# Optimization experiments

Measured on AMD Instinct MI355X. Metric: run time of the kernel, lower is better.

The kernel has to match this reference:

```python
import jax, jax.numpy as jnp
import numpy as np

N, I, H = 16, 128, 128
B, T = 16, 512


def setup_inputs() -> dict:
    key = jax.random.key(0)
    ks = jax.random.split(key, 6)
    stdv = 1.0 / np.sqrt(H)
    return {
        "x": jax.random.normal(ks[0], (B, T, N * I), dtype=jnp.float32),
        "h_0": jax.random.normal(ks[1], (1, B, N * H), dtype=jnp.float32),
        "weight_ih": jax.random.uniform(ks[2], (N, 3 * H, I), jnp.float32, -stdv, stdv),
        "weight_hh": jax.random.uniform(ks[3], (N, 3 * H, H), jnp.float32, -stdv, stdv),
        "bias_ih": jax.random.uniform(ks[4], (N, 3 * H), jnp.float32, -stdv, stdv),
        "bias_hh": jax.random.uniform(ks[5], (N, 3 * H), jnp.float32, -stdv, stdv),
    }


def reference(x, h_0, weight_ih, weight_hh, bias_ih, bias_hh):
    # x: [B, T, N*I] (batch_first)
    b, t, _ = x.shape
    xr = x.reshape(b, t, N, I)
    # Pre-compute all input projections: [B, T, N, 3H]
    gates_x = jnp.einsum('btni,ngi->btng', xr, weight_ih) + bias_ih[None, None]
    h0 = h_0[0].reshape(b, N, H)  # [B, N, H]

    def step(h, gx):
        # h: [B, N, H]; gx: [B, N, 3H]
        gates_h = jnp.einsum('bnh,ngh->bng', h, weight_hh) + bias_hh[None]
        gx_r, gx_z, gx_n = jnp.split(gx, 3, axis=-1)
        gh_r, gh_z, gh_n = jnp.split(gates_h, 3, axis=-1)
        r = jax.nn.sigmoid(gx_r + gh_r)
        z = jax.nn.sigmoid(gx_z + gh_z)
        n = jnp.tanh(gx_n + r * gh_n)
        h_new = (1 - z) * n + z * h
        return h_new, h_new

    # scan over time: gates_x -> [T, B, N, 3H]
    h_last, hs = jax.lax.scan(step, h0, jnp.swapaxes(gates_x, 0, 1))
    output = jnp.swapaxes(hs, 0, 1).reshape(b, t, N * H)  # [B, T, N*H]
    h_n = h_last.reshape(1, b, N * H)
    return output, h_n
```

## Files before the change

### kernel.cpp

```cpp
#include <hip/hip_runtime.h>
#include <cstdint>
#include <cmath>

#define N_HEADS 16
#define I_DIM 128
#define H_DIM 128
#define B_SZ 16
#define T_SZ 512
#define G3 384
#define OUT_HN_OFFSET ((size_t)B_SZ * T_SZ * (N_HEADS * H_DIM))
#define CHUNK 8
#define NCHUNK (T_SZ / CHUNK)
#define HPAD 160

typedef __attribute__((ext_vector_type(8))) short bf16x8;
typedef __attribute__((ext_vector_type(4))) float f32x4;

static __device__ __forceinline__ unsigned short f2bf(float f) {
  unsigned int u = __float_as_uint(f);
  unsigned int r = (u + 0x7FFFu + ((u >> 16) & 1u)) >> 16;
  return (unsigned short)r;
}
static __device__ __forceinline__ float bf2f(unsigned short s) {
  return __uint_as_float((unsigned int)s << 16);
}
static __device__ __forceinline__ uint2 pack4(float4 v) {
  uint2 p;
  p.x = (unsigned int)f2bf(v.x) | ((unsigned int)f2bf(v.y) << 16);
  p.y = (unsigned int)f2bf(v.z) | ((unsigned int)f2bf(v.w) << 16);
  return p;
}
static __device__ __forceinline__ bf16x8 pack8(float4 a, float4 b) {
  union { uint2 u[2]; bf16x8 v; } r;
  r.u[0] = pack4(a);
  r.u[1] = pack4(b);
  return r.v;
}

__global__ __launch_bounds__(256, 1) void gru_fused_kernel(
    const float* __restrict__ x, const float* __restrict__ h0,
    const float* __restrict__ w_ih, const float* __restrict__ w_hh,
    const float* __restrict__ b_ih, const float* __restrict__ b_hh,
    float* __restrict__ out) {
  const int b = blockIdx.x >> 4;
  const int n = blockIdx.x & 15;
  const int tid = threadIdx.x;
  const int wave = tid >> 6;
  const int lane = tid & 63;
  const int m16 = lane & 15;
  const int quad = lane >> 4;

  __shared__ __align__(16) unsigned short h2[2][2][HPAD];
  __shared__ __align__(16) float gbuf[2][CHUNK][512];

  bf16x8 wf[6][4];
  {
    const int cb0 = 2 * wave;
    const int cbs[6] = {cb0, 8 + cb0, 16 + cb0, cb0 + 1, 9 + cb0, 17 + cb0};
#pragma unroll
    for (int j = 0; j < 6; ++j) {
      const int g = cbs[j] * 16 + m16;
      const float4* wr = (const float4*)(w_hh + ((size_t)n * G3 + g) * H_DIM);
#pragma unroll
      for (int kt = 0; kt < 4; ++kt)
        wf[j][kt] = pack8(wr[kt * 8 + quad * 2], wr[kt * 8 + quad * 2 + 1]);
    }
  }

  bf16x8 wxf[6][4];
#pragma unroll
  for (int jj = 0; jj < 6; ++jj) {
    const int g = (wave * 6 + jj) * 16 + m16;
    const float4* wr = (const float4*)(w_ih + ((size_t)n * G3 + g) * I_DIM);
#pragma unroll
    for (int kt = 0; kt < 4; ++kt)
      wxf[jj][kt] = pack8(wr[kt * 8 + quad * 2], wr[kt * 8 + quad * 2 + 1]);
  }

  const bool upd = quad < 2;
  const int elem = wave * 32 + quad * 16 + m16;

  float bs_r = 0.f, bs_z = 0.f, bs_n = 0.f, bh_n = 0.f, h_old = 0.f;
  if (upd) {
    bs_r = b_ih[n * G3 + elem] + b_hh[n * G3 + elem];
    bs_z = b_ih[n * G3 + elem + 128] + b_hh[n * G3 + elem + 128];
    bs_n = b_ih[n * G3 + elem + 256];
    bh_n = b_hh[n * G3 + elem + 256];
    h_old = h0[(size_t)b * 2048 + n * H_DIM + elem];
    const unsigned short hh = f2bf(h_old);
    h2[0][0][elem] = hh;
    h2[0][1][elem] = f2bf(h_old - bf2f(hh));
  }

  const float* xrow_base = x + (size_t)b * T_SZ * 2048 + n * I_DIM +
                           (size_t)(m16 & 7) * 2048 + quad * 8;

  float4 pf[8];

#define LOAD_X_CHUNK(c)                                                       \
  {                                                                           \
    const float* xr = xrow_base + (size_t)(c) * CHUNK * 2048;                 \
    _Pragma("unroll") for (int kt = 0; kt < 4; ++kt) {                        \
      pf[kt * 2] = *(const float4*)(xr + kt * 32);                            \
      pf[kt * 2 + 1] = *(const float4*)(xr + kt * 32 + 4);                    \
    }                                                                         \
  }

#define GATES_X_CHUNK(gdst)                                                   \
  {                                                                           \
    bf16x8 af[4];                                                             \
    _Pragma("unroll") for (int kt = 0; kt < 4; ++kt)                          \
        af[kt] = pack8(pf[kt * 2], pf[kt * 2 + 1]);                           \
    _Pragma("unroll") for (int jj = 0; jj < 6; ++jj) {                        \
      f32x4 a = {0.f, 0.f, 0.f, 0.f};                                         \
      _Pragma("unroll") for (int kt = 0; kt < 4; ++kt)                        \
          a = __builtin_amdgcn_mfma_f32_16x16x32_bf16(af[kt], wxf[jj][kt], a, \
                                                      0, 0, 0);               \
      if (quad < 2) {                                                         \
        const int g = (wave * 6 + jj) * 16 + m16;                             \
        const int e4 = (g & 127) * 4 + (g >> 7);                              \
        _Pragma("unroll") for (int r = 0; r < 4; ++r)                         \
            (gdst)[(quad * 4 + r) * 512 + e4] = a[r];                         \
      }                                                                       \
    }                                                                         \
  }

  LOAD_X_CHUNK(0);
  GATES_X_CHUNK(&gbuf[0][0][0]);
  LOAD_X_CHUNK(1);
  __syncthreads();

  float* out_base = out + (size_t)b * T_SZ * 2048 + n * H_DIM;
  float oreg[CHUNK];

  for (int c = 0; c < NCHUNK; ++c) {
    const int gb = c & 1;

    if (c + 1 < NCHUNK) {
      GATES_X_CHUNK(&gbuf[gb ^ 1][0][0]);
      if (c + 2 < NCHUNK) LOAD_X_CHUNK(c + 2);
    }

#pragma unroll
    for (int s = 0; s < CHUNK; ++s) {
      const int rb = s & 1;
      const int wb = rb ^ 1;

      float gxr = 0.f, gxz = 0.f, gxn = 0.f;
      if (upd) {
        const f32x4 g4 = *(const f32x4*)&gbuf[gb][s][elem * 4];
        gxr = g4[0];
        gxz = g4[1];
        gxn = g4[2];
      }

      const unsigned short* hsrc = &h2[rb][m16 & 1][0];
      const bf16x8 av0 = *(const bf16x8*)&hsrc[0 * 32 + quad * 8];
      const bf16x8 av1 = *(const bf16x8*)&hsrc[1 * 32 + quad * 8];
      const bf16x8 av2 = *(const bf16x8*)&hsrc[2 * 32 + quad * 8];
      const bf16x8 av3 = *(const bf16x8*)&hsrc[3 * 32 + quad * 8];

      f32x4 acc[6];
#pragma unroll
      for (int j = 0; j < 6; ++j) acc[j] = (f32x4){0.f, 0.f, 0.f, 0.f};
#pragma unroll
      for (int j = 0; j < 6; ++j)
        acc[j] = __builtin_amdgcn_mfma_f32_16x16x32_bf16(av0, wf[j][0], acc[j],
                                                         0, 0, 0);
#pragma unroll
      for (int j = 0; j < 6; ++j)
        acc[j] = __builtin_amdgcn_mfma_f32_16x16x32_bf16(av1, wf[j][1], acc[j],
                                                         0, 0, 0);
#pragma unroll
      for (int j = 0; j < 6; ++j)
        acc[j] = __builtin_amdgcn_mfma_f32_16x16x32_bf16(av2, wf[j][2], acc[j],
                                                         0, 0, 0);
#pragma unroll
      for (int j = 0; j < 6; ++j)
        acc[j] = __builtin_amdgcn_mfma_f32_16x16x32_bf16(av3, wf[j][3], acc[j],
                                                         0, 0, 0);

      if (upd) {
        const float ghr =
            (quad ? acc[3][0] + acc[3][1] : acc[0][0] + acc[0][1]);
        const float ghz =
            (quad ? acc[4][0] + acc[4][1] : acc[1][0] + acc[1][1]);
        const float ghn0 =
            (quad ? acc[5][0] + acc[5][1] : acc[2][0] + acc[2][1]);
        const float r = 1.f / (1.f + __expf(-(gxr + ghr + bs_r)));
        const float z = 1.f / (1.f + __expf(-(gxz + ghz + bs_z)));
        const float targ = gxn + bs_n + r * (ghn0 + bh_n);
        const float rt = 1.f / (1.f + __expf(-2.f * targ));
        const float nn = 2.f * rt - 1.f;
        const float hn = (1.f - z) * nn + z * h_old;
        const unsigned short hh = f2bf(hn);
        h2[wb][0][elem] = hh;
        h2[wb][1][elem] = f2bf(hn - bf2f(hh));
        h_old = hn;
        oreg[s] = hn;
      }
      __syncthreads();
    }

    if (upd) {
#pragma unroll
      for (int s = 0; s < CHUNK; ++s)
        out_base[(size_t)(c * CHUNK + s) * 2048 + elem] = oreg[s];
    }
  }

  if (upd) {
    out[OUT_HN_OFFSET + (size_t)b * 2048 + n * H_DIM + elem] = h_old;
  }
}

extern "C" void kernel_launch(void* const* d_in, const int* in_sizes, int n_in,
                              void* d_out, int out_size, void* d_ws,
                              size_t ws_size, hipStream_t stream) {
  const float* x    = (const float*)d_in[0];
  const float* h0   = (const float*)d_in[1];
  const float* w_ih = (const float*)d_in[2];
  const float* w_hh = (const float*)d_in[3];
  const float* b_ih = (const float*)d_in[4];
  const float* b_hh = (const float*)d_in[5];
  float* out = (float*)d_out;
  (void)d_ws;

  gru_fused_kernel<<<256, 256, 0, stream>>>(x, h0, w_ih, w_hh, b_ih, b_hh,
                                            out);
}
```

Baseline: 431.6 us.

## Interleave input-projection MFMAs into recurrent steps and use full 16-row tiles

The time chunk grows from 8 to 16 steps, so each input-projection MFMA now uses all 16 rows of the tile instead of duplicating 8. The six projection groups for the next chunk are no longer computed in one burst at the chunk start. Instead they are spread across the first six recurrent steps, issued after the hidden-state MFMAs, so they can fill idle time on the serial critical path. The gate buffer rows are padded to 520 floats to reduce LDS bank conflicts. The cost is a larger shared buffer and more live registers (16 outputs per chunk), which may put pressure on the register file.

After: 446.8 us. 1.04x slower.

```diff
diff --git a/kernel.cpp b/kernel.cpp
--- a/kernel.cpp
+++ b/kernel.cpp
@@ -9,9 +9,10 @@
 #define T_SZ 512
 #define G3 384
 #define OUT_HN_OFFSET ((size_t)B_SZ * T_SZ * (N_HEADS * H_DIM))
-#define CHUNK 8
+#define CHUNK 16
 #define NCHUNK (T_SZ / CHUNK)
 #define HPAD 160
+#define GROWP 520
 
 typedef __attribute__((ext_vector_type(8))) short bf16x8;
 typedef __attribute__((ext_vector_type(4))) float f32x4;
@@ -51,7 +52,7 @@
   const int quad = lane >> 4;
 
   __shared__ __align__(16) unsigned short h2[2][2][HPAD];
-  __shared__ __align__(16) float gbuf[2][CHUNK][512];
+  __shared__ __align__(16) float gbuf[2][CHUNK][GROWP];
 
   bf16x8 wf[6][4];
   {
@@ -93,9 +94,10 @@
   }
 
   const float* xrow_base = x + (size_t)b * T_SZ * 2048 + n * I_DIM +
-                           (size_t)(m16 & 7) * 2048 + quad * 8;
+                           (size_t)m16 * 2048 + quad * 8;
 
   float4 pf[8];
+  bf16x8 af[4];
 
 #define LOAD_X_CHUNK(c)                                                       \
   {                                                                           \
@@ -106,27 +108,35 @@
     }                                                                         \
   }
 
-#define GATES_X_CHUNK(gdst)                                                   \
+#define PACK_AF()                                                             \
   {                                                                           \
-    bf16x8 af[4];                                                             \
     _Pragma("unroll") for (int kt = 0; kt < 4; ++kt)                          \
         af[kt] = pack8(pf[kt * 2], pf[kt * 2 + 1]);                           \
-    _Pragma("unroll") for (int jj = 0; jj < 6; ++jj) {                        \
-      f32x4 a = {0.f, 0.f, 0.f, 0.f};                                         \
-      _Pragma("unroll") for (int kt = 0; kt < 4; ++kt)                        \
-          a = __builtin_amdgcn_mfma_f32_16x16x32_bf16(af[kt], wxf[jj][kt], a, \
-                                                      0, 0, 0);               \
-      if (quad < 2) {                                                         \
-        const int g = (wave * 6 + jj) * 16 + m16;                             \
-        const int e4 = (g & 127) * 4 + (g >> 7);                              \
-        _Pragma("unroll") for (int r = 0; r < 4; ++r)                         \
-            (gdst)[(quad * 4 + r) * 512 + e4] = a[r];                         \
-      }                                                                       \
-    }                                                                         \
+  }
+
+#define GATES_X_GROUP(jj, gdst)                                               \
+  {                                                                           \
+    f32x4 a = {0.f, 0.f, 0.f, 0.f};                                           \
+    a = __builtin_amdgcn_mfma_f32_16x16x32_bf16(af[0], wxf[jj][0], a, 0, 0, 0);\
+    a = __builtin_amdgcn_mfma_f32_16x16x32_bf16(af[1], wxf[jj][1], a, 0, 0, 0);\
+    a = __builtin_amdgcn_mfma_f32_16x16x32_bf16(af[2], wxf[jj][2], a, 0, 0, 0);\
+    a = __builtin_amdgcn_mfma_f32_16x16x32_bf16(af[3], wxf[jj][3], a, 0, 0, 0);\
+    const int g_ = (wave * 6 + (jj)) * 16 + m16;                              \
+    const int e4_ = (g_ & 127) * 4 + (g_ >> 7);                               \
+    (gdst)[(quad * 4 + 0) * GROWP + e4_] = a[0];                              \
+    (gdst)[(quad * 4 + 1) * GROWP + e4_] = a[1];                              \
+    (gdst)[(quad * 4 + 2) * GROWP + e4_] = a[2];                              \
+    (gdst)[(quad * 4 + 3) * GROWP + e4_] = a[3];                              \
   }
 
   LOAD_X_CHUNK(0);
-  GATES_X_CHUNK(&gbuf[0][0][0]);
+  PACK_AF();
+  GATES_X_GROUP(0, &gbuf[0][0][0]);
+  GATES_X_GROUP(1, &gbuf[0][0][0]);
+  GATES_X_GROUP(2, &gbuf[0][0][0]);
+  GATES_X_GROUP(3, &gbuf[0][0][0]);
+  GATES_X_GROUP(4, &gbuf[0][0][0]);
+  GATES_X_GROUP(5, &gbuf[0][0][0]);
   LOAD_X_CHUNK(1);
   __syncthreads();
 
@@ -137,7 +147,7 @@
     const int gb = c & 1;
 
     if (c + 1 < NCHUNK) {
-      GATES_X_CHUNK(&gbuf[gb ^ 1][0][0]);
+      PACK_AF();
       if (c + 2 < NCHUNK) LOAD_X_CHUNK(c + 2);
     }
 
@@ -179,6 +189,10 @@
       for (int j = 0; j < 6; ++j)
         acc[j] = __builtin_amdgcn_mfma_f32_16x16x32_bf16(av3, wf[j][3], acc[j],
                                                          0, 0, 0);
+
+      if (s < 6 && c + 1 < NCHUNK) {
+        GATES_X_GROUP(s, &gbuf[gb ^ 1][0][0]);
+      }
 
       if (upd) {
         const float ghr =
```
